# Kernel tuning notes

Measured on AMD Instinct MI355X. Metric: run time of the kernel, lower is better.

The kernel has to match this reference:

```python
import jax, jax.numpy as jnp
import numpy as np
from jax import lax

WS = 0.1  # brevitas SignedBinaryWeightPerTensorConst scaling constant

def bq(w):
    # signed binary weight quant (sign * const scale) with straight-through estimator
    return w + lax.stop_gradient(WS * jnp.where(w >= 0, 1.0, -1.0) - w)

def bact(x):
    # QuantHardTanh with SignedBinaryActPerTensorConst (scale 1.0): clamp then binarize (STE)
    y = jnp.clip(x, -1.0, 1.0)
    return y + lax.stop_gradient(jnp.where(y >= 0, 1.0, -1.0) - y)

def conv1d(x, wq, b, dil):
    # x: [N,C,L], wq: [O,I,K] (already quantized), VALID padding, stride 1, rhs dilation
    y = lax.conv_general_dilated(x, wq, window_strides=(1,), padding='VALID',
                                 rhs_dilation=(dil,), dimension_numbers=('NCH', 'OIH', 'NCH'))
    return y + b[None, :, None]

def mp(x, k, p):
    # MaxPool1d(kernel=k, stride=k, padding=p)
    return lax.reduce_window(x, -jnp.inf, lax.max, (1, 1, k), (1, 1, k),
                             ((0, 0), (0, 0), (p, p)))

def sb(x, w, b):
    # QuantScaleBias: per-channel binary-quantized scale + float bias
    return x * bq(w)[None, :, None] + b[None, :, None]

def setup_inputs() -> dict:
    key = jax.random.key(0)
    ks = jax.random.split(key, 32)
    C, D = 256, 8
    def n(k, shape, s=1.0):
        return jax.random.normal(k, shape, jnp.float32) * s
    inp = {"x": n(ks[0], (128, 3, 2560))}
    specs = [(3, C, 23), (C, C, 13), (C, C, 7), (C, C, 5), (C, C, 5), (C, D, 3)]
    i = 1
    for li, (ci, co, k) in enumerate(specs, start=1):
        inp[f"w{li}"] = n(ks[i], (co, ci, k), 0.1)
        inp[f"b{li}"] = n(ks[i + 1], (co,), 0.01)
        inp[f"sw{li}"] = n(ks[i + 2], (co,))
        inp[f"sb{li}"] = n(ks[i + 3], (co,), 0.01)
        i += 4
    inp["fw1"] = n(ks[25], (512, 32), 0.1)
    inp["fsw1"] = n(ks[26], (512,))
    inp["fsb1"] = n(ks[27], (512,), 0.01)
    inp["fw2"] = n(ks[28], (1000, 512), 0.1)
    inp["fsw2"] = n(ks[29], (1000,))
    inp["fsb2"] = n(ks[30], (1000,), 0.01)
    return inp

def reference(x, w1, b1, sw1, sb1, w2, b2, sw2, sb2, w3, b3, sw3, sb3,
              w4, b4, sw4, sb4, w5, b5, sw5, sb5, w6, b6, sw6, sb6,
              fw1, fsw1, fsb1, fw2, fsw2, fsb2):
    x = bact(sb(mp(conv1d(x, bq(w1), b1, 7), 5, 2), sw1, sb1))  # L: 2560->2406->482
    x = bact(sb(mp(conv1d(x, bq(w2), b2, 3), 3, 1), sw2, sb2))  # ->446->149
    x = bact(sb(mp(conv1d(x, bq(w3), b3, 2), 3, 1), sw3, sb3))  # ->137->46
    x = bact(sb(conv1d(x, bq(w4), b4, 1), sw4, sb4))            # ->42
    x = bact(sb(mp(conv1d(x, bq(w5), b5, 1), 3, 1), sw5, sb5))  # ->38->13
    x = bact(sb(mp(conv1d(x, bq(w6), b6, 1), 3, 1), sw6, sb6))  # ->11->4, C=8
    x = x.reshape(-1, 32)  # depth * embedding_factor = 8*4
    x = x @ bq(fw1).T
    x = bact(x * bq(fsw1) + fsb1)
    x = x @ bq(fw2).T
    return x * bq(fsw2) + fsb2
```

## Files before the change

### kernel.cpp

```cpp
#include <hip/hip_runtime.h>
#include <cstdint>
#include <cstddef>

typedef unsigned long long u64;
typedef uint32_t u32;
typedef uint16_t u16;
typedef uint8_t u8;
typedef __attribute__((ext_vector_type(8))) short bf16x8;
typedef __attribute__((ext_vector_type(4))) float f32x4;


#define CONV1_MARGIN 1e-4f

struct PackJob { const float* src; u64* dst; int Cout, CIN, K, waveBase; };
struct PackJobs {
    PackJob j[6]; int totalWaves;
    const float* fw1; u32* fw1pk;
    const float* w1;  u16* wbf;
};

__global__ void pack_all_kernel(PackJobs P)
{
    int gtid = blockIdx.x * blockDim.x + threadIdx.x;
    int wid = gtid >> 6, lane = gtid & 63;
    if (wid < P.totalWaves) {
        int jj = 0;
        #pragma unroll
        for (int i = 1; i < 6; ++i) if (wid >= P.j[i].waveBase) jj = i;
        PackJob job = P.j[jj];
        int lw = wid - job.waveBase;
        int W = job.CIN >> 6;
        int wg = lw % W;
        int co = (lw / W) % job.Cout;
        int k  = lw / (W * job.Cout);
        int ci = wg * 64 + lane;
        bool sg = job.src[((size_t)co * job.CIN + ci) * job.K + k] >= 0.0f;
        u64 word = __ballot(sg);
        if (lane == 0) job.dst[lw] = word;
        return;
    }
    int idx = gtid - P.totalWaves * 64;
    if (idx < 512) {
        u32 wd = 0;
        #pragma unroll
        for (int i = 0; i < 32; ++i) wd |= (u32)(P.fw1[idx * 32 + i] >= 0.0f) << i;
        P.fw1pk[idx] = wd;
    }
    int j = idx - 512;
    if (j >= 0 && j < 256 * 192) {
        int co = j / 192, k = j - co * 192;
        int i = (k >= 96) ? (k - 96) : k;
        u16 val = 0;
        if (i < 69)
            val = (P.w1[(size_t)co * 69 + i] >= 0.0f) ? (u16)0x3F80 : (u16)0xBF80;
        P.wbf[(size_t)co * 192 + k] = val;
    }
}

__global__ __launch_bounds__(256) void conv1_mfma_kernel(
    const float* __restrict__ x, const u16* __restrict__ wbf,
    const float* __restrict__ b, const float* __restrict__ sw,
    const float* __restrict__ sb,
    u64* __restrict__ opk64, u64* __restrict__ uflag64)
{
    __shared__ u16 Xb[16 * 208];
    __shared__ unsigned poolm[128 * 16];
    const int Lconv = 2406, Lin = 2560;
    int n = blockIdx.x, T = blockIdx.y, ch = blockIdx.z;
    int tid = threadIdx.x, lane = tid & 63, w = tid >> 6;
    int l0 = 80 * T - 2;

    for (int i = tid; i < 128 * 16; i += 256) poolm[i] = 0u;

    bf16x8 afr[2][6];
    {
        int cobase = 128 * ch + 32 * w;
        #pragma unroll
        for (int m = 0; m < 2; ++m) {
            const u16* wp = wbf + (size_t)(cobase + m * 16 + (lane & 15)) * 192
                           + (lane >> 4) * 8;
            #pragma unroll
            for (int s = 0; s < 6; ++s)
                afr[m][s] = *(const bf16x8*)(wp + s * 32);
        }
    }

    const float* xb = x + (size_t)n * 3 * Lin;

    for (int j = 0; j < 5; ++j) {
        __syncthreads();
        #pragma unroll
        for (int e = 0; e < 6; ++e) {
            int elem = tid + 256 * e;
            int p = elem & 15, i = elem >> 4;
            u16 hi = 0, lo = 0;
            if (i < 69) {
                int ci = (i < 23) ? 0 : ((i < 46) ? 1 : 2);
                int kk = i - 23 * ci;
                int l = l0 + 16 * j + p + 7 * kk;
                int c = min(max(l, 0), Lin - 1);
                float xv = xb[ci * Lin + c];
                u32 ub = __float_as_uint(xv);
                u32 h = (ub + 0x7FFFu + ((ub >> 16) & 1u)) >> 16;
                hi = (u16)h;
                float rem = xv - __uint_as_float(h << 16);
                u32 ur = __float_as_uint(rem);
                lo = (u16)((ur + 0x7FFFu + ((ur >> 16) & 1u)) >> 16);
            }
            Xb[p * 208 + i] = hi;
            Xb[p * 208 + 96 + i] = lo;
        }
        __syncthreads();

        f32x4 acc0 = {0.0f, 0.0f, 0.0f, 0.0f};
        f32x4 acc1 = {0.0f, 0.0f, 0.0f, 0.0f};
        const u16* brow = &Xb[(lane & 15) * 208 + (lane >> 4) * 8];
        #pragma unroll
        for (int s = 0; s < 6; ++s) {
            bf16x8 bf = *(const bf16x8*)(brow + s * 32);
            acc0 = __builtin_amdgcn_mfma_f32_16x16x32_bf16(afr[0][s], bf, acc0, 0, 0, 0);
            acc1 = __builtin_amdgcn_mfma_f32_16x16x32_bf16(afr[1][s], bf, acc1, 0, 0, 0);
        }

        int p = lane & 15;
        int q = 16 * j + p;
        int l = l0 + q;
        if (l >= 0 && l < Lconv) {
            int lp_loc = q / 5;
            #pragma unroll
            for (int m = 0; m < 2; ++m) {
                #pragma unroll
                for (int r = 0; r < 4; ++r) {
                    float v = (m == 0) ? acc0[r] : acc1[r];
                    int co_loc = 32 * w + 16 * m + (lane >> 4) * 4 + r;
                    u32 bits = __float_as_uint(v);
                    u32 mv = (bits & 0x80000000u) ? ~bits : (bits | 0x80000000u);
                    atomicMax(&poolm[co_loc * 16 + lp_loc], mv);
                }
            }
        }
    }
    __syncthreads();

    {
        int co_loc = tid & 127;
        int half = tid >> 7;
        int co = 128 * ch + co_loc;
        float bc = b[co];
        float swc = (sw[co] >= 0.0f) ? 0.1f : -0.1f;
        float sbc = sb[co];
        #pragma unroll
        for (int k = 0; k < 8; ++k) {
            int lp_loc = half * 8 + k;
            int lp = 16 * T + lp_loc;
            bool bit = false, unc = false;
            if (lp < 482) {
                u32 mv = poolm[co_loc * 16 + lp_loc];
                u32 bits = (mv & 0x80000000u) ? (mv & 0x7FFFFFFFu) : ~mv;
                float best = __uint_as_float(bits);
                float v = swc * (0.1f * best + bc) + sbc;
                bit = (v >= 0.0f);
                unc = (fabsf(v) < CONV1_MARGIN);
            }
            u64 wb = __ballot(bit);
            u64 wu = __ballot(unc);
            if (lp < 482 && lane == 0) {
                size_t widx = ((size_t)n * 482 + lp) * 4 + (ch * 2 + (co_loc >> 6));
                opk64[widx] = wb;
                uflag64[widx] = wu;
            }
        }
    }
}

__global__ void conv1_fixup_kernel(const float* __restrict__ x,
                                   const float* __restrict__ w1,
                                   const float* __restrict__ b,
                                   const float* __restrict__ sw,
                                   const float* __restrict__ sb,
                                   const u64* __restrict__ uflag64,
                                   u64* __restrict__ opk64)
{
    int idx = blockIdx.x * blockDim.x + threadIdx.x;
    if (idx >= 128 * 482 * 4) return;
    u64 f = uflag64[idx];
    if (f == 0) return;
    int og = idx & 3;
    int lp = (idx >> 2) % 482;
    int n = idx / (4 * 482);
    u64 word = opk64[idx];
    const float* xb = x + (size_t)n * 3 * 2560;
    while (f) {
        int c = __ffsll(f) - 1;
        f &= f - 1;
        int co = og * 64 + c;
        const float* wp = w1 + (size_t)co * 69;
        double best = -1e300;
        for (int t = 0; t < 5; ++t) {
            int gl = 5 * lp - 2 + t;
            if (gl < 0 || gl >= 2406) continue;
            double s = 0.0;
            #pragma unroll
            for (int ci = 0; ci < 3; ++ci) {
                const float* xp = xb + ci * 2560 + gl;
                const float* wq = wp + ci * 23;
                #pragma unroll
                for (int kk = 0; kk < 23; ++kk) {
                    double xv = (double)xp[kk * 7];
                    s += (wq[kk] >= 0.0f) ? xv : -xv;
                }
            }
            best = fmax(best, s);
        }
        double v = ((sw[co] >= 0.0f) ? 0.1 : -0.1) * (0.1 * best + (double)b[co]) + (double)sb[co];
        u64 bit = (v >= 0.0) ? 1ull : 0ull;
        word = (word & ~(1ull << c)) | (bit << c);
    }
    opk64[idx] = word;
}

template<int K, int DIL, int PK, int PP, int W, int LPW>
__global__ void bconv_bit_kernel(const u64* __restrict__ apk,
                                 const u64* __restrict__ wpk,
                                 const float* __restrict__ b,
                                 const float* __restrict__ sw,
                                 const float* __restrict__ sb,
                                 u64* __restrict__ opk,
                                 int Cout, int Lin, int Lconv, int Lout,
                                 int NLPG, int nwaves)
{
    int wid = __builtin_amdgcn_readfirstlane(
        (int)(blockIdx.x * (blockDim.x >> 6)) + (int)(threadIdx.x >> 6));
    int lane = threadIdx.x & 63;
    if (wid >= nwaves) return;
    int WOUT = Cout >> 6;
    int og = wid % WOUT;
    int lpg = (wid / WOUT) % NLPG;
    int n  = wid / (WOUT * NLPG);
    int lp0 = lpg * LPW;
    int co = og * 64 + lane;

    const u64* ab = apk + (size_t)n * Lin * W;
    int cnt[LPW][PK];
    #pragma unroll
    for (int j = 0; j < LPW; ++j)
        #pragma unroll
        for (int t = 0; t < PK; ++t) cnt[j][t] = 0;

    #pragma unroll
    for (int k = 0; k < K; ++k) {
        u64 ww[W];
        #pragma unroll
        for (int w = 0; w < W; ++w)
            ww[w] = wpk[((size_t)k * Cout + co) * W + w];
        #pragma unroll
        for (int j = 0; j < LPW; ++j) {
            int lp = lp0 + j;
            #pragma unroll
            for (int t = 0; t < PK; ++t) {
                int l = lp * PK - PP + t;
                if (lp >= Lout || l < 0 || l >= Lconv) continue;
                const u64* ap = ab + (size_t)(l + k * DIL) * W;
                #pragma unroll
                for (int w = 0; w < W; ++w)
                    cnt[j][t] += __popcll(ap[w] ^ ww[w]);
            }
        }
    }
    const int CINK = W * 64 * K;
    #pragma unroll
    for (int j = 0; j < LPW; ++j) {
        int lp = lp0 + j;
        int best = -2147483647;
        #pragma unroll
        for (int t = 0; t < PK; ++t) {
            int l = lp * PK - PP + t;
            if (l < 0 || l >= Lconv) continue;
            int ksum = CINK - 2 * cnt[j][t];
            best = (ksum > best) ? ksum : best;
        }
        bool bit = false;
        if (lp < Lout) {
            double conv = 0.1 * (double)best + (double)b[co];
            double v = ((sw[co] >= 0.0f) ? 0.1 : -0.1) * conv + (double)sb[co];
            bit = (v >= 0.0);
        }
        u64 word = __ballot(bit);
        if (lp < Lout && lane == 0)
            opk[((size_t)n * Lout + lp) * WOUT + og] = word;
    }
}

__global__ __launch_bounds__(256) void tail_kernel(
    const u64* __restrict__ a3,
    const u64* __restrict__ wpk4,
    const u64* __restrict__ wpk5,
    const u64* __restrict__ wpk6,
    const float* __restrict__ b4, const float* __restrict__ sw4, const float* __restrict__ sb4,
    const float* __restrict__ b5, const float* __restrict__ sw5, const float* __restrict__ sb5,
    const float* __restrict__ b6, const float* __restrict__ sw6, const float* __restrict__ sb6,
    const u32* __restrict__ fw1pk,
    const float* __restrict__ fsw1, const float* __restrict__ fsb1,
    const u64* __restrict__ fpk2,
    const float* __restrict__ fsw2, const float* __restrict__ fsb2,
    float* __restrict__ out)
{
    __shared__ u64 sA[46 * 4];
    __shared__ u64 sB[42 * 4];
    __shared__ u64 sC[13 * 4];
    __shared__ u32 sA6;
    __shared__ u64 sH[8];
    int n = blockIdx.x, tid = threadIdx.x, lane = tid & 63, wv = tid >> 6;

    for (int i = tid; i < 46 * 4; i += 256) sA[i] = a3[(size_t)n * 46 * 4 + i];
    __syncthreads();

    {
        u64 ww[5][4];
        #pragma unroll
        for (int k = 0; k < 5; ++k)
            #pragma unroll
            for (int w = 0; w < 4; ++w)
                ww[k][w] = wpk4[((size_t)k * 256 + tid) * 4 + w];
        double bc = b4[tid];
        double swc = (sw4[tid] >= 0.0f) ? 0.1 : -0.1;
        double sbc = sb4[tid];
        for (int lp = 0; lp < 42; ++lp) {
            int cnt = 0;
            #pragma unroll
            for (int k = 0; k < 5; ++k)
                #pragma unroll
                for (int w = 0; w < 4; ++w)
                    cnt += __popcll(sA[(lp + k) * 4 + w] ^ ww[k][w]);
            int ksum = 256 * 5 - 2 * cnt;
            double v = swc * (0.1 * ksum + bc) + sbc;
            u64 word = __ballot(v >= 0.0);
            if (lane == 0) sB[lp * 4 + wv] = word;
        }
    }
    __syncthreads();

    {
        u64 ww[5][4];
        #pragma unroll
        for (int k = 0; k < 5; ++k)
            #pragma unroll
            for (int w = 0; w < 4; ++w)
                ww[k][w] = wpk5[((size_t)k * 256 + tid) * 4 + w];
        double bc = b5[tid];
        double swc = (sw5[tid] >= 0.0f) ? 0.1 : -0.1;
        double sbc = sb5[tid];
        for (int lp = 0; lp < 13; ++lp) {
            int best = -2147483647;
            #pragma unroll
            for (int t = 0; t < 3; ++t) {
                int l = 3 * lp - 1 + t;
                if (l < 0 || l >= 38) continue;
                int cnt = 0;
                #pragma unroll
                for (int k = 0; k < 5; ++k)
                    #pragma unroll
                    for (int w = 0; w < 4; ++w)
                        cnt += __popcll(sB[(l + k) * 4 + w] ^ ww[k][w]);
                int ksum = 256 * 5 - 2 * cnt;
                best = (ksum > best) ? ksum : best;
            }
            double v = swc * (0.1 * best + bc) + sbc;
            u64 word = __ballot(v >= 0.0);
            if (lane == 0) sC[lp * 4 + wv] = word;
        }
    }
    __syncthreads();

    if (tid < 32) {
        int co = tid >> 2, lp = tid & 3;
        int best = -2147483647;
        for (int t = 0; t < 3; ++t) {
            int l = 3 * lp - 1 + t;
            if (l < 0 || l >= 11) continue;
            int cnt = 0;
            #pragma unroll
            for (int k = 0; k < 3; ++k)
                #pragma unroll
                for (int w = 0; w < 4; ++w)
                    cnt += __popcll(sC[(l + k) * 4 + w] ^ wpk6[((size_t)k * 8 + co) * 4 + w]);
            int ksum = 256 * 3 - 2 * cnt;
            best = (ksum > best) ? ksum : best;
        }
        double v = ((sw6[co] >= 0.0f) ? 0.1 : -0.1) * (0.1 * best + (double)b6[co]) + (double)sb6[co];
        u64 word = __ballot(v >= 0.0);
        if (tid == 0) sA6 = (u32)word;
    }
    __syncthreads();

    {
        u32 a6w = sA6;
        #pragma unroll
        for (int p = 0; p < 2; ++p) {
            int o = tid + p * 256;
            int k = 32 - 2 * __popc(a6w ^ fw1pk[o]);
            double v = ((fsw1[o] >= 0.0f) ? 0.1 : -0.1) * (0.1 * (double)k) + (double)fsb1[o];
            u64 word = __ballot(v >= 0.0);
            if (lane == 0) sH[p * 4 + wv] = word;
        }
    }
    __syncthreads();

    {
        u64 h[8];
        #pragma unroll
        for (int w = 0; w < 8; ++w) h[w] = sH[w];
        #pragma unroll
        for (int p = 0; p < 4; ++p) {
            int o = tid + p * 256;
            if (o < 1000) {
                int cnt = 0;
                #pragma unroll
                for (int w = 0; w < 8; ++w)
                    cnt += __popcll(h[w] ^ fpk2[(size_t)o * 8 + w]);
                int k = 512 - 2 * cnt;
                double v = ((fsw2[o] >= 0.0f) ? 0.1 : -0.1) * (0.1 * (double)k) + (double)fsb2[o];
                out[(size_t)n * 1000 + o] = (float)v;
            }
        }
    }
}

extern "C" void kernel_launch(void* const* d_in, const int* in_sizes, int n_in,
                              void* d_out, int out_size, void* d_ws, size_t ws_size,
                              hipStream_t stream) {
    const float* x = (const float*)d_in[0];
    const float *w[6], *b[6], *sw[6], *sb[6];
    for (int i = 0; i < 6; ++i) {
        w[i]  = (const float*)d_in[1 + 4 * i];
        b[i]  = (const float*)d_in[2 + 4 * i];
        sw[i] = (const float*)d_in[3 + 4 * i];
        sb[i] = (const float*)d_in[4 + 4 * i];
    }
    const float* fw1  = (const float*)d_in[25];
    const float* fsw1 = (const float*)d_in[26];
    const float* fsb1 = (const float*)d_in[27];
    const float* fw2  = (const float*)d_in[28];
    const float* fsw2 = (const float*)d_in[29];
    const float* fsb2 = (const float*)d_in[30];
    float* out = (float*)d_out;
    (void)in_sizes; (void)n_in; (void)out_size; (void)ws_size;

    char* wsbase = (char*)d_ws;
    size_t off = 0;
    auto alloc = [&](size_t bytes) -> char* {
        char* p = wsbase + off;
        off = (off + bytes + 255) & ~(size_t)255;
        return p;
    };
    u64* wpk2 = (u64*)alloc((size_t)13 * 256 * 4 * 8);
    u64* wpk3 = (u64*)alloc((size_t)7 * 256 * 4 * 8);
    u64* wpk4 = (u64*)alloc((size_t)5 * 256 * 4 * 8);
    u64* wpk5 = (u64*)alloc((size_t)5 * 256 * 4 * 8);
    u64* wpk6 = (u64*)alloc((size_t)3 * 8 * 4 * 8);
    u64* fpk2 = (u64*)alloc((size_t)1000 * 8 * 8);
    u32* fw1pk = (u32*)alloc((size_t)512 * 4);
    u16* wbf = (u16*)alloc((size_t)256 * 192 * 2);
    u64* uflag64 = (u64*)alloc((size_t)128 * 482 * 4 * 8);
    u64* a1   = (u64*)alloc((size_t)128 * 482 * 4 * 8);
    u64* a2   = (u64*)alloc((size_t)128 * 149 * 4 * 8);
    u64* a3   = (u64*)alloc((size_t)128 * 46 * 4 * 8);

    const int BLK = 256;
    auto blocksForWaves = [](int nwaves) { return dim3((unsigned)((nwaves * 64 + 255) / 256)); };
    auto blocksForThreads = [](int n) { return dim3((unsigned)((n + 255) / 256)); };

    {
        PackJobs P;
        int base = 0;
        auto setJob = [&](int i, const float* src, u64* dst, int Cout, int CIN, int K) {
            P.j[i] = {src, dst, Cout, CIN, K, base};
            base += K * Cout * (CIN >> 6);
        };
        setJob(0, w[1], wpk2, 256, 256, 13);
        setJob(1, w[2], wpk3, 256, 256, 7);
        setJob(2, w[3], wpk4, 256, 256, 5);
        setJob(3, w[4], wpk5, 256, 256, 5);
        setJob(4, w[5], wpk6, 8, 256, 3);
        setJob(5, fw2, fpk2, 1000, 512, 1);
        P.totalWaves = base;
        P.fw1 = fw1; P.fw1pk = fw1pk; P.w1 = w[0]; P.wbf = wbf;
        int totalThreads = base * 64 + 512 + 256 * 192;
        pack_all_kernel<<<blocksForThreads(totalThreads), BLK, 0, stream>>>(P);
    }

    conv1_mfma_kernel<<<dim3(128, 31, 2), BLK, 0, stream>>>(
        x, wbf, b[0], sw[0], sb[0], a1, uflag64);
    conv1_fixup_kernel<<<blocksForThreads(128 * 482 * 4), BLK, 0, stream>>>(
        x, w[0], b[0], sw[0], sb[0], uflag64, a1);

    {
        const int NLPG = (149 + 3) / 4;
        int nw = 128 * NLPG * 4;
        bconv_bit_kernel<13, 3, 3, 1, 4, 4><<<blocksForWaves(nw), BLK, 0, stream>>>(
            a1, wpk2, b[1], sw[1], sb[1], a2, 256, 482, 446, 149, NLPG, nw);
    }
    {
        const int NLPG = (46 + 3) / 4;
        int nw = 128 * NLPG * 4;
        bconv_bit_kernel<7, 2, 3, 1, 4, 4><<<blocksForWaves(nw), BLK, 0, stream>>>(
            a2, wpk3, b[2], sw[2], sb[2], a3, 256, 149, 137, 46, NLPG, nw);
    }
    tail_kernel<<<dim3(128), BLK, 0, stream>>>(
        a3, wpk4, wpk5, wpk6,
        b[3], sw[3], sb[3], b[4], sw[4], sb[4], b[5], sw[5], sb[5],
        fw1pk, fsw1, fsb1, fpk2, fsw2, fsb2, out);
}
```

Measured before the change: 349.2 us.

## Stage conv1 input once in LDS and replace atomic max-pool with buffered reduction

```diff
diff --git a/kernel.cpp b/kernel.cpp
--- a/kernel.cpp
+++ b/kernel.cpp
@@ -63,15 +63,14 @@
     const float* __restrict__ sb,
     u64* __restrict__ opk64, u64* __restrict__ uflag64)
 {
-    __shared__ u16 Xb[16 * 208];
-    __shared__ unsigned poolm[128 * 16];
+    __shared__ u32 xhl[3 * 236];
+    __shared__ u32 Xb32[16 * 108];
+    __shared__ float poolf[128 * 81];
     const int Lconv = 2406, Lin = 2560;
     int n = blockIdx.x, T = blockIdx.y, ch = blockIdx.z;
     int tid = threadIdx.x, lane = tid & 63, w = tid >> 6;
     int l0 = 80 * T - 2;
 
-    for (int i = tid; i < 128 * 16; i += 256) poolm[i] = 0u;
-
     bf16x8 afr[2][6];
     {
         int cobase = 128 * ch + 32 * w;
@@ -86,35 +85,49 @@
     }
 
     const float* xb = x + (size_t)n * 3 * Lin;
+    #pragma unroll
+    for (int e = 0; e < 3; ++e) {
+        int idx = tid + 256 * e;
+        if (idx < 3 * 236) {
+            int ci = idx / 236, lrel = idx - ci * 236;
+            int l = min(max(l0 + lrel, 0), Lin - 1);
+            float xv = xb[ci * Lin + l];
+            u32 ub = __float_as_uint(xv);
+            u32 h = (ub + 0x7FFFu + ((ub >> 16) & 1u)) >> 16;
+            float rem = xv - __uint_as_float(h << 16);
+            u32 ur = __float_as_uint(rem);
+            u32 lo = (ur + 0x7FFFu + ((ur >> 16) & 1u)) >> 16;
+            xhl[idx] = (h & 0xFFFFu) | (lo << 16);
+        }
+    }
+    __syncthreads();
 
     for (int j = 0; j < 5; ++j) {
-        __syncthreads();
-        #pragma unroll
-        for (int e = 0; e < 6; ++e) {
-            int elem = tid + 256 * e;
-            int p = elem & 15, i = elem >> 4;
-            u16 hi = 0, lo = 0;
-            if (i < 69) {
-                int ci = (i < 23) ? 0 : ((i < 46) ? 1 : 2);
-                int kk = i - 23 * ci;
-                int l = l0 + 16 * j + p + 7 * kk;
-                int c = min(max(l, 0), Lin - 1);
-                float xv = xb[ci * Lin + c];
-                u32 ub = __float_as_uint(xv);
-                u32 h = (ub + 0x7FFFu + ((ub >> 16) & 1u)) >> 16;
-                hi = (u16)h;
-                float rem = xv - __uint_as_float(h << 16);
-                u32 ur = __float_as_uint(rem);
-                lo = (u16)((ur + 0x7FFFu + ((ur >> 16) & 1u)) >> 16);
-            }
-            Xb[p * 208 + i] = hi;
-            Xb[p * 208 + 96 + i] = lo;
+        if (j) __syncthreads();
+        #pragma unroll
+        for (int e = 0; e < 3; ++e) {
+            int s = tid + 256 * e;
+            int p = s & 15, i2 = s >> 4;
+            u32 hiw = 0, low = 0;
+            #pragma unroll
+            for (int t2 = 0; t2 < 2; ++t2) {
+                int t = 2 * i2 + t2;
+                if (t < 69) {
+                    int ci = (t < 23) ? 0 : ((t < 46) ? 1 : 2);
+                    int kk = t - 23 * ci;
+                    u32 v = xhl[ci * 236 + 16 * j + p + 7 * kk];
+                    hiw |= (v & 0xFFFFu) << (16 * t2);
+                    low |= (v >> 16) << (16 * t2);
+                }
+            }
+            Xb32[p * 108 + i2] = hiw;
+            Xb32[p * 108 + 48 + i2] = low;
         }
         __syncthreads();
 
         f32x4 acc0 = {0.0f, 0.0f, 0.0f, 0.0f};
         f32x4 acc1 = {0.0f, 0.0f, 0.0f, 0.0f};
-        const u16* brow = &Xb[(lane & 15) * 208 + (lane >> 4) * 8];
+        const u16* brow = (const u16*)Xb32 + (lane & 15) * 216 + (lane >> 4) * 8;
         #pragma unroll
         for (int s = 0; s < 6; ++s) {
             bf16x8 bf = *(const bf16x8*)(brow + s * 32);
@@ -122,53 +135,46 @@
             acc1 = __builtin_amdgcn_mfma_f32_16x16x32_bf16(afr[1][s], bf, acc1, 0, 0, 0);
         }
 
-        int p = lane & 15;
-        int q = 16 * j + p;
-        int l = l0 + q;
-        if (l >= 0 && l < Lconv) {
-            int lp_loc = q / 5;
-            #pragma unroll
-            for (int m = 0; m < 2; ++m) {
-                #pragma unroll
-                for (int r = 0; r < 4; ++r) {
-                    float v = (m == 0) ? acc0[r] : acc1[r];
-                    int co_loc = 32 * w + 16 * m + (lane >> 4) * 4 + r;
-                    u32 bits = __float_as_uint(v);
-                    u32 mv = (bits & 0x80000000u) ? ~bits : (bits | 0x80000000u);
-                    atomicMax(&poolm[co_loc * 16 + lp_loc], mv);
-                }
-            }
-        }
-    }
-    __syncthreads();
-
-    {
-        int co_loc = tid & 127;
-        int half = tid >> 7;
+        int q = 16 * j + (lane & 15);
+        #pragma unroll
+        for (int m = 0; m < 2; ++m) {
+            #pragma unroll
+            for (int r = 0; r < 4; ++r) {
+                float v = (m == 0) ? acc0[r] : acc1[r];
+                int co_loc = 32 * w + 16 * m + (lane >> 4) * 4 + r;
+                poolf[co_loc * 81 + q] = v;
+            }
+        }
+    }
+    __syncthreads();
+
+    #pragma unroll
+    for (int it = 0; it < 8; ++it) {
+        int idx = tid + 256 * it;
+        int co_loc = idx & 127;
+        int lp_loc = idx >> 7;
+        int lp = 16 * T + lp_loc;
         int co = 128 * ch + co_loc;
-        float bc = b[co];
-        float swc = (sw[co] >= 0.0f) ? 0.1f : -0.1f;
-        float sbc = sb[co];
-        #pragma unroll
-        for (int k = 0; k < 8; ++k) {
-            int lp_loc = half * 8 + k;
-            int lp = 16 * T + lp_loc;
-            bool bit = false, unc = false;
-            if (lp < 482) {
-                u32 mv = poolm[co_loc * 16 + lp_loc];
-                u32 bits = (mv & 0x80000000u) ? (mv & 0x7FFFFFFFu) : ~mv;
-                float best = __uint_as_float(bits);
-                float v = swc * (0.1f * best + bc) + sbc;
-                bit = (v >= 0.0f);
-                unc = (fabsf(v) < CONV1_MARGIN);
-            }
-            u64 wb = __ballot(bit);
-            u64 wu = __ballot(unc);
-            if (lp < 482 && lane == 0) {
-                size_t widx = ((size_t)n * 482 + lp) * 4 + (ch * 2 + (co_loc >> 6));
-                opk64[widx] = wb;
-                uflag64[widx] = wu;
-            }
+        bool bit = false, unc = false;
+        if (lp < 482) {
+            float best = -1e30f;
+            #pragma unroll
+            for (int t = 0; t < 5; ++t) {
+                int q = 5 * lp_loc + t;
+                int l = l0 + q;
+                if (l >= 0 && l < Lconv)
+                    best = fmaxf(best, poolf[co_loc * 81 + q]);
+            }
+            float v = ((sw[co] >= 0.0f) ? 0.1f : -0.1f) * (0.1f * best + b[co]) + sb[co];
+            bit = (v >= 0.0f);
+            unc = (fabsf(v) < CONV1_MARGIN);
+        }
+        u64 wb = __ballot(bit);
+        u64 wu = __ballot(unc);
+        if (lp < 482 && lane == 0) {
+            size_t widx = ((size_t)n * 482 + lp) * 4 + (ch * 2 + (co_loc >> 6));
+            opk64[widx] = wb;
+            uflag64[widx] = wu;
         }
     }
 }
```

New measurement: 314.7 us. -9.9%, faster.
